# Performance work log

Measured on AMD Instinct MI355X. Metric: run time of the kernel, lower is better.

Reference implementation:

```python
import jax, jax.numpy as jnp
import numpy as np

B = 16          # batch
DF = 1536       # dinov2 feature dim
D = 1024        # projected dim (32*32)
V = 6890        # SMPL vertices (hard-coded in DECO)
PD = 256        # vertex positional-embedding dim
HID = 512       # feature_transform hidden dim
C = 133         # semantic contact classes


def setup_inputs() -> dict:
    key = jax.random.key(0)
    ks = jax.random.split(key, 16)
    s = 0.02
    n = lambda k, shp: s * jax.random.normal(k, shp, dtype=jnp.float32)
    return {
        "features": jax.random.normal(ks[0], (B, DF), dtype=jnp.float32),
        "W_scene": n(ks[1], (DF, D)), "b_scene": jnp.zeros((D,), jnp.float32),
        "W_contact": n(ks[2], (DF, D)), "b_contact": jnp.zeros((D,), jnp.float32),
        "Wq": n(ks[3], (D, D)), "Wk": n(ks[4], (D, D)),
        "Wv": n(ks[5], (D, D)), "Wo": n(ks[6], (D, D)),
        "W_cls": n(ks[7], (D, V)), "b_cls": jnp.zeros((V,), jnp.float32),
        "pos_emb": n(ks[8], (V, PD)),
        "W_ft1": n(ks[9], (D + PD, HID)), "b_ft1": jnp.zeros((HID,), jnp.float32),
        "W_ft2": n(ks[10], (HID, C)), "b_ft2": jnp.zeros((C,), jnp.float32),
    }


def reference(features, W_scene, b_scene, W_contact, b_contact,
              Wq, Wk, Wv, Wo, W_cls, b_cls, pos_emb,
              W_ft1, b_ft1, W_ft2, b_ft2):
    b = features.shape[0]
    # projectors (dinov2 branch)
    sem = features @ W_scene + b_scene          # [B, D]
    part = features @ W_contact + b_contact     # [B, D]
    # cross attention over seq-len-1 tokens: q from sem, k/v from part
    q = (sem @ Wq)[:, None, :]                  # [B, 1, D]
    k = (part @ Wk)[:, None, :]
    v = (part @ Wv)[:, None, :]
    scores = jnp.einsum('bqd,bkd->bqk', q, k) / jnp.sqrt(jnp.float32(D))
    w = jax.nn.softmax(scores, axis=-1)
    att = jnp.einsum('bqk,bkd->bqd', w, v) @ Wo  # [B, 1, D]
    # per-vertex contact probability
    cont = jax.nn.sigmoid(att[:, 0, :] @ W_cls + b_cls)  # [B, V]
    # shared semantic classifier: the torch code loops over batches, does
    # nonzero() on (cont > 0.5), gathers pos embeddings for contact vertices,
    # runs feature_transform, and scatters into zeros(B, C, V). The masked
    # vectorized form below computes identical values.
    mask = cont > 0.5                           # [B, V] (int constant wrt grad)
    att_bv = jnp.broadcast_to(att, (b, V, D))   # att[b] repeated per vertex
    pos_bv = jnp.broadcast_to(pos_emb[None], (b, V, PD))
    combined = jnp.concatenate([att_bv, pos_bv], axis=-1)   # [B, V, D+PD]
    h = jax.nn.relu(combined @ W_ft1 + b_ft1)   # [B, V, HID]
    preds = h @ W_ft2 + b_ft2                   # [B, V, C]
    semantic_cont = jnp.where(mask[:, None, :],
                              jnp.transpose(preds, (0, 2, 1)),
                              jnp.float32(0.0))  # [B, C, V]
    return (cont, semantic_cont)
```

## Files before the change

kernel.cpp:

```cpp
#include <hip/hip_runtime.h>
#include <hip/hip_bf16.h>

#define B_   16
#define DF_  1536
#define D_   1024
#define V_   6890
#define PD_  256
#define HID_ 512
#define C_   133
#define VPAD 6912
#define CPAD 144

typedef short short8 __attribute__((ext_vector_type(8)));
typedef float float4_ __attribute__((ext_vector_type(4)));
typedef unsigned short ushort_t;

#define MFMA16 __builtin_amdgcn_mfma_f32_16x16x32_bf16

__device__ __forceinline__ float b2f(ushort_t u) {
  union { unsigned int i; float f; } x;
  x.i = ((unsigned int)u) << 16;
  return x.f;
}
__device__ __forceinline__ ushort_t f2b(float f) {
  union { float f; unsigned int i; } x;
  x.f = f;
  unsigned int r = (x.i + 0x7fffu + ((x.i >> 16) & 1u)) >> 16;
  return (ushort_t)r;
}
__device__ __forceinline__ unsigned int f22u(float h0, float h1) {
  __hip_bfloat162 hb = __float22bfloat162_rn(make_float2(h0, h1));
  unsigned int u;
  __builtin_memcpy(&u, &hb, sizeof(u));
  return u;
}

__global__ __launch_bounds__(256) void k_gemv_fA(const float* __restrict__ A,
                                                 const float* __restrict__ W,
                                                 const float* __restrict__ bias,
                                                 double* __restrict__ outd,
                                                 float* __restrict__ outf,
                                                 int K, int N) {
  __shared__ double sA[DF_];
  int b = blockIdx.y;
  for (int i = threadIdx.x; i < K; i += 256) sA[i] = (double)A[b * K + i];
  __syncthreads();
  int jl = threadIdx.x & 15, ks = threadIdx.x >> 4;
  int j  = blockIdx.x * 16 + jl;
  int klen = K >> 4;
  const double* Ar = sA + ks * klen;
  const float*  Wp = W + (size_t)(ks * klen) * N + j;
  double acc = 0.0;
#pragma unroll 8
  for (int kk = 0; kk < klen; ++kk)
    acc += Ar[kk] * (double)Wp[(size_t)kk * N];
  __shared__ double red[16][16];
  red[ks][jl] = acc;
  __syncthreads();
  if (threadIdx.x < 16) {
    int jj = blockIdx.x * 16 + threadIdx.x;
    double s = 0.0;
#pragma unroll
    for (int q = 0; q < 16; ++q) s += red[q][threadIdx.x];
    if (bias) s += (double)bias[jj];
    if (outd) outd[b * N + jj] = s;
    if (outf) outf[b * N + jj] = (float)s;
  }
}

__global__ __launch_bounds__(256) void k_gemv_dA(const double* __restrict__ A,
                                                 const float* __restrict__ W,
                                                 const float* __restrict__ bias,
                                                 double* __restrict__ outd,
                                                 float* __restrict__ outf,
                                                 int K, int N) {
  __shared__ double sA[D_];
  int b = blockIdx.y;
  for (int i = threadIdx.x; i < K; i += 256) sA[i] = A[b * K + i];
  __syncthreads();
  int jl = threadIdx.x & 15, ks = threadIdx.x >> 4;
  int j  = blockIdx.x * 16 + jl;
  int klen = K >> 4;
  const double* Ar = sA + ks * klen;
  const float*  Wp = W + (size_t)(ks * klen) * N + j;
  double acc = 0.0;
#pragma unroll 8
  for (int kk = 0; kk < klen; ++kk)
    acc += Ar[kk] * (double)Wp[(size_t)kk * N];
  __shared__ double red[16][16];
  red[ks][jl] = acc;
  __syncthreads();
  if (threadIdx.x < 16) {
    int jj = blockIdx.x * 16 + threadIdx.x;
    double s = 0.0;
#pragma unroll
    for (int q = 0; q < 16; ++q) s += red[q][threadIdx.x];
    if (bias) s += (double)bias[jj];
    if (outd) outd[b * N + jj] = s;
    if (outf) outf[b * N + jj] = (float)s;
  }
}

__global__ __launch_bounds__(256) void k_cont(const double* __restrict__ att,
                                              const float* __restrict__ Wcls,
                                              const float* __restrict__ bcls,
                                              unsigned char* __restrict__ maskb,
                                              float* __restrict__ out0) {
  int vl = threadIdx.x & 15, ks = threadIdx.x >> 4;
  int v  = blockIdx.x * 16 + vl;
  int vc = v < V_ ? v : V_ - 1;
  double acc[B_];
#pragma unroll
  for (int b = 0; b < B_; ++b) acc[b] = 0.0;
  int k0 = ks * 64;
#pragma unroll 8
  for (int kk = 0; kk < 64; ++kk) {
    int k = k0 + kk;
    double w = (double)Wcls[(size_t)k * V_ + vc];
#pragma unroll
    for (int b = 0; b < B_; ++b) acc[b] += att[b * D_ + k] * w;
  }
  __shared__ double red[16][B_][16];
#pragma unroll
  for (int b = 0; b < B_; ++b) red[ks][b][vl] = acc[b];
  __syncthreads();
  int b = threadIdx.x >> 4;
  double s = 0.0;
#pragma unroll
  for (int q = 0; q < 16; ++q) s += red[q][b][vl];
  if (v < V_) {
    s += (double)bcls[v];
    maskb[b * V_ + v] = (s > 0.0) ? 1 : 0;
    out0[b * V_ + v] = (float)(1.0 / (1.0 + exp(-s)));
  }
}

__global__ __launch_bounds__(256) void k_prep(const float* __restrict__ Wft2,
                                              const float* __restrict__ Wft1,
                                              const float* __restrict__ pos,
                                              ushort_t* __restrict__ WT,
                                              ushort_t* __restrict__ WbT,
                                              ushort_t* __restrict__ PB) {
  int i = blockIdx.x * 256 + threadIdx.x;
  if (i < CPAD * HID_) {
    int c = i >> 9, k = i & (HID_ - 1);
    WT[i] = (c < C_) ? f2b(Wft2[(size_t)k * C_ + c]) : (ushort_t)0;
    return;
  }
  i -= CPAD * HID_;
  if (i < HID_ * PD_) {
    int k = i & (HID_ - 1), pd = i >> 9;
    WbT[(size_t)k * PD_ + pd] = f2b(Wft1[(size_t)(D_ + pd) * HID_ + k]);
    return;
  }
  i -= HID_ * PD_;
  if (i < V_ * PD_) PB[i] = f2b(pos[i]);
}

__global__ __launch_bounds__(256) void k_pproj(const ushort_t* __restrict__ PB,
                                               const ushort_t* __restrict__ WbT,
                                               ushort_t* __restrict__ PP) {
  int wave = threadIdx.x >> 6, lane = threadIdx.x & 63;
  int q = lane >> 4, l15 = lane & 15;
  int m0 = blockIdx.x * 64 + wave * 16;
  int n0 = blockIdx.y * 64;
  int vc = m0 + l15; vc = vc < V_ ? vc : V_ - 1;
  const ushort_t* pb = PB + (size_t)vc * PD_;
  float4_ acc[4] = {};
#pragma unroll 2
  for (int kt = 0; kt < 8; ++kt) {
    int jb = kt * 32 + q * 8;
    short8 a = *(const short8*)(pb + jb);
#pragma unroll
    for (int nf = 0; nf < 4; ++nf) {
      int n = n0 + nf * 16 + l15;
      short8 bfr = *(const short8*)(WbT + (size_t)n * PD_ + jb);
      acc[nf] = MFMA16(a, bfr, acc[nf], 0, 0, 0);
    }
  }
  int v0w = m0 + q * 4;
#pragma unroll
  for (int nf = 0; nf < 4; ++nf)
#pragma unroll
    for (int r = 0; r < 4; ++r)
      PP[(size_t)(v0w + r) * HID_ + (n0 + nf * 16 + l15)] = f2b(acc[nf][r]);
}

__global__ __launch_bounds__(256, 2) void k_main(const ushort_t* __restrict__ WT,
                                                 const ushort_t* __restrict__ PP,
                                                 const float* __restrict__ attproj,
                                                 const unsigned char* __restrict__ maskb,
                                                 const float* __restrict__ bft2,
                                                 float* __restrict__ out1) {
  __shared__ ushort_t swt[2][CPAD * 32];
  __shared__ float attp[2][HID_];
  int b0 = blockIdx.y * 2;
  int wave = threadIdx.x >> 6, lane = threadIdx.x & 63;
  int q = lane >> 4, l15 = lane & 15;
  int vbase = blockIdx.x * 128 + wave * 32;

  for (int i = threadIdx.x; i < 2 * HID_; i += 256)
    attp[i >> 9][i & (HID_ - 1)] = attproj[(b0 + (i >> 9)) * HID_ + (i & (HID_ - 1))];

  auto stage = [&](int kt, int buf) {
#pragma unroll
    for (int ii = 0; ii < 3; ++ii) {
      int i = ii * 256 + threadIdx.x;
      if (i < 576) {
        int row = i >> 2, seg = i & 3;
        *(short8*)&swt[buf][row * 32 + seg * 8] =
            *(const short8*)(WT + (size_t)row * HID_ + kt * 32 + seg * 8);
      }
    }
  };
  stage(0, 0);

  const ushort_t* pbase0 = PP + (size_t)(vbase + l15) * HID_;
  const ushort_t* pbase1 = PP + (size_t)(vbase + 16 + l15) * HID_;
  short8 pcur[2];
  pcur[0] = *(const short8*)(pbase0 + q * 8);
  pcur[1] = *(const short8*)(pbase1 + q * 8);
  __syncthreads();

  float4_ acc[2][9][2] = {};
  for (int kt = 0; kt < 16; ++kt) {
    int buf = kt & 1;
    int kb = kt * 32 + q * 8;
    if (kt < 15) stage(kt + 1, buf ^ 1);
    short8 pnext[2] = {pcur[0], pcur[1]};
    if (kt < 15) {
      pnext[0] = *(const short8*)(pbase0 + kb + 32);
      pnext[1] = *(const short8*)(pbase1 + kb + 32);
    }
    float pf[2][8];
#pragma unroll
    for (int nf = 0; nf < 2; ++nf)
#pragma unroll
      for (int jj = 0; jj < 8; ++jj)
        pf[nf][jj] = b2f((ushort_t)pcur[nf][jj]);
    float af[2][8];
#pragma unroll
    for (int bb = 0; bb < 2; ++bb) {
      float4_ a0 = *(const float4_*)&attp[bb][kb];
      float4_ a1 = *(const float4_*)&attp[bb][kb + 4];
#pragma unroll
      for (int e = 0; e < 4; ++e) { af[bb][e] = a0[e]; af[bb][4 + e] = a1[e]; }
    }
    short8 bfr[2][2];
#pragma unroll
    for (int bb = 0; bb < 2; ++bb)
#pragma unroll
      for (int nf = 0; nf < 2; ++nf) {
        unsigned int uu[4];
#pragma unroll
        for (int jj = 0; jj < 8; jj += 2) {
          float h0 = af[bb][jj]     + pf[nf][jj];
          float h1 = af[bb][jj + 1] + pf[nf][jj + 1];
          h0 = h0 > 0.f ? h0 : 0.f;
          h1 = h1 > 0.f ? h1 : 0.f;
          uu[jj >> 1] = f22u(h0, h1);
        }
        __builtin_memcpy(&bfr[bb][nf], uu, 16);
      }
#pragma unroll
    for (int mt = 0; mt < 9; ++mt) {
      short8 a = *(const short8*)&swt[buf][(mt * 16 + l15) * 32 + q * 8];
      acc[0][mt][0] = MFMA16(a, bfr[0][0], acc[0][mt][0], 0, 0, 0);
      acc[0][mt][1] = MFMA16(a, bfr[0][1], acc[0][mt][1], 0, 0, 0);
      acc[1][mt][0] = MFMA16(a, bfr[1][0], acc[1][mt][0], 0, 0, 0);
      acc[1][mt][1] = MFMA16(a, bfr[1][1], acc[1][mt][1], 0, 0, 0);
    }
    pcur[0] = pnext[0];
    pcur[1] = pnext[1];
    __syncthreads();
  }

  bool mk[2][2];
  int  nn[2];
#pragma unroll
  for (int nf = 0; nf < 2; ++nf) {
    int n = vbase + nf * 16 + l15;
    nn[nf] = n;
    int ncl = n < V_ ? n : V_ - 1;
    mk[0][nf] = (n < V_) && (maskb[(b0 + 0) * V_ + ncl] != 0);
    mk[1][nf] = (n < V_) && (maskb[(b0 + 1) * V_ + ncl] != 0);
  }
#pragma unroll
  for (int bb = 0; bb < 2; ++bb) {
    float* ob = out1 + (size_t)(b0 + bb) * C_ * V_;
#pragma unroll
    for (int mt = 0; mt < 9; ++mt)
#pragma unroll
      for (int r = 0; r < 4; ++r) {
        int c = mt * 16 + q * 4 + r;
        if (c < C_) {
          float bias = bft2[c];
#pragma unroll
          for (int nf = 0; nf < 2; ++nf)
            if (nn[nf] < V_) {
              float val = mk[bb][nf] ? acc[bb][mt][nf][r] + bias : 0.f;
              ob[(size_t)c * V_ + nn[nf]] = val;
            }
        }
      }
  }
}

extern "C" void kernel_launch(void* const* d_in, const int* in_sizes, int n_in,
                              void* d_out, int out_size, void* d_ws, size_t ws_size,
                              hipStream_t stream) {
  const float* features  = (const float*)d_in[0];
  const float* W_contact = (const float*)d_in[3];
  const float* b_contact = (const float*)d_in[4];
  const float* Wv        = (const float*)d_in[7];
  const float* Wo        = (const float*)d_in[8];
  const float* W_cls     = (const float*)d_in[9];
  const float* b_cls     = (const float*)d_in[10];
  const float* pos_emb   = (const float*)d_in[11];
  const float* W_ft1     = (const float*)d_in[12];
  const float* b_ft1     = (const float*)d_in[13];
  const float* W_ft2     = (const float*)d_in[14];
  const float* b_ft2     = (const float*)d_in[15];

  char* ws = (char*)d_ws;
  double*        part  = (double*)(ws);
  unsigned char* maskb = (unsigned char*)(ws);
  double*        vv    = (double*)(ws + 131072);
  double*        att   = (double*)(ws + 262144);
  float*         attpj = (float*)(ws + 393216);
  ushort_t*      wt    = (ushort_t*)(ws + 425984);
  ushort_t*      wbt   = (ushort_t*)(ws + 573440);
  ushort_t*      pp    = (ushort_t*)(ws + 835584);
  ushort_t*      pb    = (ushort_t*)(ws + 7913472);

  float* out0 = (float*)d_out;
  float* out1 = out0 + (size_t)B_ * V_;

  k_prep<<<7690, 256, 0, stream>>>(W_ft2, W_ft1, pos_emb, wt, wbt, pb);
  k_pproj<<<dim3(108, 8), 256, 0, stream>>>(pb, wbt, pp);
  k_gemv_fA<<<dim3(64, 16), 256, 0, stream>>>(features, W_contact, b_contact, part, nullptr, DF_, D_);
  k_gemv_dA<<<dim3(64, 16), 256, 0, stream>>>(part, Wv, nullptr, vv, nullptr, D_, D_);
  k_gemv_dA<<<dim3(64, 16), 256, 0, stream>>>(vv, Wo, nullptr, att, nullptr, D_, D_);
  k_gemv_dA<<<dim3(32, 16), 256, 0, stream>>>(att, W_ft1, b_ft1, nullptr, attpj, D_, HID_);
  k_cont<<<432, 256, 0, stream>>>(att, W_cls, b_cls, maskb, out0);
  k_main<<<dim3(54, 8), 256, 0, stream>>>(wt, pp, attpj, maskb, b_ft2, out1);
}
```

Measured before the change: 266.3 us.

## Batch GEMVs across all rows with split-K atomics and fuse sigmoid into main

The fp64 GEMV kernels now compute all 16 batch rows per block, so each weight element is read once instead of once per batch row. K is split across grid.y, with partial sums added into buffers that a prep kernel pre-initialises with the biases. The pos_emb bf16 conversion moves into the projection kernel through a swizzled LDS tile, which removes a global round trip. The contact classifier accumulates logits with atomics, and the sigmoid and mask are computed in k_main. The cost is fp64 atomic contention, non-deterministic summation order, and much smaller grids of 64 blocks for the GEMVs.

```diff
diff --git a/kernel.cpp b/kernel.cpp
--- a/kernel.cpp
+++ b/kernel.cpp
@@ -8,7 +8,6 @@
 #define PD_  256
 #define HID_ 512
 #define C_   133
-#define VPAD 6912
 #define CPAD 144
 
 typedef short short8 __attribute__((ext_vector_type(8)));
@@ -35,112 +34,13 @@
   return u;
 }
 
-__global__ __launch_bounds__(256) void k_gemv_fA(const float* __restrict__ A,
-                                                 const float* __restrict__ W,
-                                                 const float* __restrict__ bias,
-                                                 double* __restrict__ outd,
-                                                 float* __restrict__ outf,
-                                                 int K, int N) {
-  __shared__ double sA[DF_];
-  int b = blockIdx.y;
-  for (int i = threadIdx.x; i < K; i += 256) sA[i] = (double)A[b * K + i];
-  __syncthreads();
-  int jl = threadIdx.x & 15, ks = threadIdx.x >> 4;
-  int j  = blockIdx.x * 16 + jl;
-  int klen = K >> 4;
-  const double* Ar = sA + ks * klen;
-  const float*  Wp = W + (size_t)(ks * klen) * N + j;
-  double acc = 0.0;
-#pragma unroll 8
-  for (int kk = 0; kk < klen; ++kk)
-    acc += Ar[kk] * (double)Wp[(size_t)kk * N];
-  __shared__ double red[16][16];
-  red[ks][jl] = acc;
-  __syncthreads();
-  if (threadIdx.x < 16) {
-    int jj = blockIdx.x * 16 + threadIdx.x;
-    double s = 0.0;
-#pragma unroll
-    for (int q = 0; q < 16; ++q) s += red[q][threadIdx.x];
-    if (bias) s += (double)bias[jj];
-    if (outd) outd[b * N + jj] = s;
-    if (outf) outf[b * N + jj] = (float)s;
-  }
-}
-
-__global__ __launch_bounds__(256) void k_gemv_dA(const double* __restrict__ A,
-                                                 const float* __restrict__ W,
-                                                 const float* __restrict__ bias,
-                                                 double* __restrict__ outd,
-                                                 float* __restrict__ outf,
-                                                 int K, int N) {
-  __shared__ double sA[D_];
-  int b = blockIdx.y;
-  for (int i = threadIdx.x; i < K; i += 256) sA[i] = A[b * K + i];
-  __syncthreads();
-  int jl = threadIdx.x & 15, ks = threadIdx.x >> 4;
-  int j  = blockIdx.x * 16 + jl;
-  int klen = K >> 4;
-  const double* Ar = sA + ks * klen;
-  const float*  Wp = W + (size_t)(ks * klen) * N + j;
-  double acc = 0.0;
-#pragma unroll 8
-  for (int kk = 0; kk < klen; ++kk)
-    acc += Ar[kk] * (double)Wp[(size_t)kk * N];
-  __shared__ double red[16][16];
-  red[ks][jl] = acc;
-  __syncthreads();
-  if (threadIdx.x < 16) {
-    int jj = blockIdx.x * 16 + threadIdx.x;
-    double s = 0.0;
-#pragma unroll
-    for (int q = 0; q < 16; ++q) s += red[q][threadIdx.x];
-    if (bias) s += (double)bias[jj];
-    if (outd) outd[b * N + jj] = s;
-    if (outf) outf[b * N + jj] = (float)s;
-  }
-}
-
-__global__ __launch_bounds__(256) void k_cont(const double* __restrict__ att,
-                                              const float* __restrict__ Wcls,
-                                              const float* __restrict__ bcls,
-                                              unsigned char* __restrict__ maskb,
-                                              float* __restrict__ out0) {
-  int vl = threadIdx.x & 15, ks = threadIdx.x >> 4;
-  int v  = blockIdx.x * 16 + vl;
-  int vc = v < V_ ? v : V_ - 1;
-  double acc[B_];
-#pragma unroll
-  for (int b = 0; b < B_; ++b) acc[b] = 0.0;
-  int k0 = ks * 64;
-#pragma unroll 8
-  for (int kk = 0; kk < 64; ++kk) {
-    int k = k0 + kk;
-    double w = (double)Wcls[(size_t)k * V_ + vc];
-#pragma unroll
-    for (int b = 0; b < B_; ++b) acc[b] += att[b * D_ + k] * w;
-  }
-  __shared__ double red[16][B_][16];
-#pragma unroll
-  for (int b = 0; b < B_; ++b) red[ks][b][vl] = acc[b];
-  __syncthreads();
-  int b = threadIdx.x >> 4;
-  double s = 0.0;
-#pragma unroll
-  for (int q = 0; q < 16; ++q) s += red[q][b][vl];
-  if (v < V_) {
-    s += (double)bcls[v];
-    maskb[b * V_ + v] = (s > 0.0) ? 1 : 0;
-    out0[b * V_ + v] = (float)(1.0 / (1.0 + exp(-s)));
-  }
-}
-
-__global__ __launch_bounds__(256) void k_prep(const float* __restrict__ Wft2,
-                                              const float* __restrict__ Wft1,
-                                              const float* __restrict__ pos,
-                                              ushort_t* __restrict__ WT,
-                                              ushort_t* __restrict__ WbT,
-                                              ushort_t* __restrict__ PB) {
+__global__ __launch_bounds__(256) void k_prep2(
+    const float* __restrict__ Wft2, const float* __restrict__ Wft1,
+    const float* __restrict__ bcon, const float* __restrict__ bft1,
+    const float* __restrict__ bcls, ushort_t* __restrict__ WT,
+    ushort_t* __restrict__ WbT, double* __restrict__ part,
+    double* __restrict__ vv, double* __restrict__ att,
+    double* __restrict__ attpjd, double* __restrict__ sbuf) {
   int i = blockIdx.x * 256 + threadIdx.x;
   if (i < CPAD * HID_) {
     int c = i >> 9, k = i & (HID_ - 1);
@@ -154,23 +54,116 @@
     return;
   }
   i -= HID_ * PD_;
-  if (i < V_ * PD_) PB[i] = f2b(pos[i]);
-}
-
-__global__ __launch_bounds__(256) void k_pproj(const ushort_t* __restrict__ PB,
+  if (i < B_ * D_) { part[i] = (double)bcon[i & (D_ - 1)]; return; }
+  i -= B_ * D_;
+  if (i < B_ * D_) { vv[i] = 0.0; return; }
+  i -= B_ * D_;
+  if (i < B_ * D_) { att[i] = 0.0; return; }
+  i -= B_ * D_;
+  if (i < B_ * HID_) { attpjd[i] = (double)bft1[i & (HID_ - 1)]; return; }
+  i -= B_ * HID_;
+  if (i < B_ * V_) { sbuf[i] = (double)bcls[i % V_]; return; }
+}
+
+__global__ __launch_bounds__(256) void k_gA(const float* __restrict__ A32,
+                                            const double* __restrict__ A64,
+                                            const float* __restrict__ W,
+                                            double* __restrict__ out,
+                                            int K, int N) {
+  __shared__ double sh[6144];
+  int KCH = K >> 2, KQ = KCH >> 2;
+  int ky0 = blockIdx.y * KCH;
+  int tid = threadIdx.x;
+  for (int i = tid; i < 16 * KCH; i += 256) {
+    int b = i / KCH, kl = i - b * KCH;
+    sh[i] = A32 ? (double)A32[(size_t)b * K + ky0 + kl]
+                : A64[(size_t)b * K + ky0 + kl];
+  }
+  __syncthreads();
+  int jl = tid & 63, ksub = tid >> 6;
+  int j = blockIdx.x * 64 + jl;
+  double acc[16];
+#pragma unroll
+  for (int b = 0; b < 16; ++b) acc[b] = 0.0;
+  const float* Wp = W + (size_t)(ky0 + ksub * KQ) * N + j;
+  const double* Ab = sh + ksub * KQ;
+#pragma unroll 4
+  for (int kk = 0; kk < KQ; ++kk) {
+    double w = (double)Wp[(size_t)kk * N];
+    const double* ap = Ab + kk;
+#pragma unroll
+    for (int b = 0; b < 16; ++b) acc[b] += ap[(size_t)b * KCH] * w;
+  }
+  __syncthreads();
+  double* red = sh;
+#pragma unroll
+  for (int b = 0; b < 16; ++b) red[(ksub * 16 + b) * 64 + jl] = acc[b];
+  __syncthreads();
+  for (int i = tid; i < 1024; i += 256) {
+    int b = i >> 6, jj = i & 63;
+    double v = red[(0 * 16 + b) * 64 + jj] + red[(1 * 16 + b) * 64 + jj] +
+               red[(2 * 16 + b) * 64 + jj] + red[(3 * 16 + b) * 64 + jj];
+    atomicAdd(&out[(size_t)b * N + blockIdx.x * 64 + jj], v);
+  }
+}
+
+__global__ __launch_bounds__(256) void k_cont2(const double* __restrict__ att,
+                                               const float* __restrict__ Wcls,
+                                               double* __restrict__ sbuf) {
+  __shared__ double sh[4096];
+  int tid = threadIdx.x;
+  int v = blockIdx.x * 64 + (tid & 63);
+  int bg = tid >> 6;
+  int vc = v < V_ ? v : V_ - 1;
+  double acc[4] = {0.0, 0.0, 0.0, 0.0};
+#pragma unroll
+  for (int ch = 0; ch < 2; ++ch) {
+    int k0 = blockIdx.y * 512 + ch * 256;
+    for (int i = tid; i < 4096; i += 256)
+      sh[i] = att[(size_t)(i >> 8) * D_ + k0 + (i & 255)];
+    __syncthreads();
+    const double* ab = sh + bg * 4 * 256;
+#pragma unroll 8
+    for (int kk = 0; kk < 256; ++kk) {
+      double w = (double)Wcls[(size_t)(k0 + kk) * V_ + vc];
+#pragma unroll
+      for (int b = 0; b < 4; ++b) acc[b] += ab[b * 256 + kk] * w;
+    }
+    __syncthreads();
+  }
+  if (v < V_)
+#pragma unroll
+    for (int b = 0; b < 4; ++b)
+      atomicAdd(&sbuf[(size_t)(bg * 4 + b) * V_ + v], acc[b]);
+}
+
+__global__ __launch_bounds__(256) void k_pproj(const float* __restrict__ pos,
                                                const ushort_t* __restrict__ WbT,
                                                ushort_t* __restrict__ PP) {
+  __shared__ ushort_t pb_lds[64 * 256];
   int wave = threadIdx.x >> 6, lane = threadIdx.x & 63;
   int q = lane >> 4, l15 = lane & 15;
-  int m0 = blockIdx.x * 64 + wave * 16;
+  int vblk = blockIdx.x * 64;
   int n0 = blockIdx.y * 64;
-  int vc = m0 + l15; vc = vc < V_ ? vc : V_ - 1;
-  const ushort_t* pb = PB + (size_t)vc * PD_;
+
+  for (int i = threadIdx.x; i < 64 * 128; i += 256) {
+    int v = i >> 7, e2 = i & 127;
+    int vc = vblk + v; vc = vc < V_ ? vc : V_ - 1;
+    const float* sp = pos + (size_t)vc * PD_ + e2 * 2;
+    unsigned int u = f22u(sp[0], sp[1]);
+    int bsw = (e2 * 4) ^ ((v & 7) << 4);
+    *(unsigned int*)((char*)pb_lds + v * 512 + bsw) = u;
+  }
+  __syncthreads();
+
+  int m0 = wave * 16;
   float4_ acc[4] = {};
 #pragma unroll 2
   for (int kt = 0; kt < 8; ++kt) {
     int jb = kt * 32 + q * 8;
-    short8 a = *(const short8*)(pb + jb);
+    int row = m0 + l15;
+    int bsw = (jb * 2) ^ ((row & 7) << 4);
+    short8 a = *(const short8*)((const char*)pb_lds + row * 512 + bsw);
 #pragma unroll
     for (int nf = 0; nf < 4; ++nf) {
       int n = n0 + nf * 16 + l15;
@@ -178,7 +171,7 @@
       acc[nf] = MFMA16(a, bfr, acc[nf], 0, 0, 0);
     }
   }
-  int v0w = m0 + q * 4;
+  int v0w = vblk + m0 + q * 4;
 #pragma unroll
   for (int nf = 0; nf < 4; ++nf)
 #pragma unroll
@@ -188,9 +181,10 @@
 
 __global__ __launch_bounds__(256, 2) void k_main(const ushort_t* __restrict__ WT,
                                                  const ushort_t* __restrict__ PP,
-                                                 const float* __restrict__ attproj,
-                                                 const unsigned char* __restrict__ maskb,
+                                                 const double* __restrict__ attpjd,
+                                                 const double* __restrict__ sbuf,
                                                  const float* __restrict__ bft2,
+                                                 float* __restrict__ out0,
                                                  float* __restrict__ out1) {
   __shared__ ushort_t swt[2][CPAD * 32];
   __shared__ float attp[2][HID_];
@@ -200,7 +194,8 @@
   int vbase = blockIdx.x * 128 + wave * 32;
 
   for (int i = threadIdx.x; i < 2 * HID_; i += 256)
-    attp[i >> 9][i & (HID_ - 1)] = attproj[(b0 + (i >> 9)) * HID_ + (i & (HID_ - 1))];
+    attp[i >> 9][i & (HID_ - 1)] =
+        (float)attpjd[(size_t)(b0 + (i >> 9)) * HID_ + (i & (HID_ - 1))];
 
   auto stage = [&](int kt, int buf) {
 #pragma unroll
@@ -282,8 +277,13 @@
     int n = vbase + nf * 16 + l15;
     nn[nf] = n;
     int ncl = n < V_ ? n : V_ - 1;
-    mk[0][nf] = (n < V_) && (maskb[(b0 + 0) * V_ + ncl] != 0);
-    mk[1][nf] = (n < V_) && (maskb[(b0 + 1) * V_ + ncl] != 0);
+#pragma unroll
+    for (int bb = 0; bb < 2; ++bb) {
+      double sv = sbuf[(size_t)(b0 + bb) * V_ + ncl];
+      mk[bb][nf] = (n < V_) && (sv > 0.0);
+      if (q == 0 && n < V_)
+        out0[(size_t)(b0 + bb) * V_ + n] = (float)(1.0 / (1.0 + exp(-sv)));
+    }
   }
 #pragma unroll
   for (int bb = 0; bb < 2; ++bb) {
@@ -323,25 +323,25 @@
   const float* b_ft2     = (const float*)d_in[15];
 
   char* ws = (char*)d_ws;
-  double*        part  = (double*)(ws);
-  unsigned char* maskb = (unsigned char*)(ws);
-  double*        vv    = (double*)(ws + 131072);
-  double*        att   = (double*)(ws + 262144);
-  float*         attpj = (float*)(ws + 393216);
-  ushort_t*      wt    = (ushort_t*)(ws + 425984);
-  ushort_t*      wbt   = (ushort_t*)(ws + 573440);
-  ushort_t*      pp    = (ushort_t*)(ws + 835584);
-  ushort_t*      pb    = (ushort_t*)(ws + 7913472);
+  double*   part   = (double*)(ws);
+  double*   vv     = (double*)(ws + 131072);
+  double*   att    = (double*)(ws + 262144);
+  double*   attpjd = (double*)(ws + 393216);
+  double*   sbuf   = (double*)(ws + 458752);
+  ushort_t* wt     = (ushort_t*)(ws + 1341440);
+  ushort_t* wbt    = (ushort_t*)(ws + 1488896);
+  ushort_t* pp     = (ushort_t*)(ws + 1751040);
 
   float* out0 = (float*)d_out;
   float* out1 = out0 + (size_t)B_ * V_;
 
-  k_prep<<<7690, 256, 0, stream>>>(W_ft2, W_ft1, pos_emb, wt, wbt, pb);
-  k_pproj<<<dim3(108, 8), 256, 0, stream>>>(pb, wbt, pp);
-  k_gemv_fA<<<dim3(64, 16), 256, 0, stream>>>(features, W_contact, b_contact, part, nullptr, DF_, D_);
-  k_gemv_dA<<<dim3(64, 16), 256, 0, stream>>>(part, Wv, nullptr, vv, nullptr, D_, D_);
-  k_gemv_dA<<<dim3(64, 16), 256, 0, stream>>>(vv, Wo, nullptr, att, nullptr, D_, D_);
-  k_gemv_dA<<<dim3(32, 16), 256, 0, stream>>>(att, W_ft1, b_ft1, nullptr, attpj, D_, HID_);
-  k_cont<<<432, 256, 0, stream>>>(att, W_cls, b_cls, maskb, out0);
-  k_main<<<dim3(54, 8), 256, 0, stream>>>(wt, pp, attpj, maskb, b_ft2, out1);
-}
+  k_prep2<<<1455, 256, 0, stream>>>(W_ft2, W_ft1, b_contact, b_ft1, b_cls,
+                                    wt, wbt, part, vv, att, attpjd, sbuf);
+  k_pproj<<<dim3(108, 8), 256, 0, stream>>>(pos_emb, wbt, pp);
+  k_gA<<<dim3(16, 4), 256, 0, stream>>>(features, nullptr, W_contact, part, DF_, D_);
+  k_gA<<<dim3(16, 4), 256, 0, stream>>>(nullptr, part, Wv, vv, D_, D_);
+  k_gA<<<dim3(16, 4), 256, 0, stream>>>(nullptr, vv, Wo, att, D_, D_);
+  k_gA<<<dim3(8, 4), 256, 0, stream>>>(nullptr, att, W_ft1, attpjd, D_, HID_);
+  k_cont2<<<dim3(108, 2), 256, 0, stream>>>(att, W_cls, sbuf);
+  k_main<<<dim3(54, 8), 256, 0, stream>>>(wt, pp, attpjd, sbuf, b_ft2, out0, out1);
+}
```

Measured after the change: 392.5 us. +47.4%, slower.
